# Performance work log

Measured on AMD Instinct MI355X. Metric: run time of the kernel, lower is better.

The kernel has to match this reference:

```python
import jax, jax.numpy as jnp
import numpy as np

N = 50000      # nodes
E = 800000     # edges (avg degree 16)
H = 128        # hidden_nf
NORM_FACTOR = 100.0   # normalization_factor, aggregation 'sum'
NORM_CONST = 1.0      # norm_constant (effective_constant = max(1, 1.0))
EPS = 1e-8


def silu(v):
    return v * jax.nn.sigmoid(v)


def setup_inputs() -> dict:
    key = jax.random.key(0)
    ks = jax.random.split(key, 16)
    IN_E = 2 * H + 2  # edge MLP input: h[row] | h[col] | [radial, edge_attr]

    def w(k, shape, scale=0.05):
        return jax.random.normal(k, shape, dtype=jnp.float32) * scale

    return {
        "h": jax.random.normal(ks[0], (N, H), dtype=jnp.float32),
        "x": jax.random.normal(ks[1], (N, 3), dtype=jnp.float32),
        "edge_index": jax.random.randint(ks[2], (2, E), 0, N, dtype=jnp.int32),
        "edge_attr": jax.random.normal(ks[3], (E, 1), dtype=jnp.float32),
        "node_mask": jnp.ones((N, 1), dtype=jnp.float32),
        "edge_mask": jnp.ones((E, 1), dtype=jnp.float32),
        # 2 stacked GCL layers (identical shapes -> stacked on leading dim)
        "gcl_e_w1": w(ks[4], (2, IN_E, H)), "gcl_e_b1": jnp.zeros((2, H), jnp.float32),
        "gcl_e_w2": w(ks[5], (2, H, H)),    "gcl_e_b2": jnp.zeros((2, H), jnp.float32),
        "gcl_a_w":  w(ks[6], (2, H, 1)),    "gcl_a_b":  jnp.zeros((2, 1), jnp.float32),
        "gcl_n_w1": w(ks[7], (2, 2 * H, H)),"gcl_n_b1": jnp.zeros((2, H), jnp.float32),
        "gcl_n_w2": w(ks[8], (2, H, H)),    "gcl_n_b2": jnp.zeros((2, H), jnp.float32),
        # EquivariantUpdate coord MLP (last layer xavier gain 0.001 -> tiny, no bias)
        "c_w1": w(ks[9], (IN_E, H)), "c_b1": jnp.zeros((H,), jnp.float32),
        "c_w2": w(ks[10], (H, H)),   "c_b2": jnp.zeros((H,), jnp.float32),
        "c_w3": w(ks[11], (H, 1), 0.001),
    }


def reference(h, x, edge_index, edge_attr, node_mask, edge_mask,
              gcl_e_w1, gcl_e_b1, gcl_e_w2, gcl_e_b2, gcl_a_w, gcl_a_b,
              gcl_n_w1, gcl_n_b1, gcl_n_w2, gcl_n_b2,
              c_w1, c_b1, c_w2, c_b2, c_w3):
    row, col = edge_index[0], edge_index[1]
    n_nodes = h.shape[0]

    # coord2diff
    diff = x[row] - x[col]                                  # [E,3]
    radial = jnp.sum(diff * diff, axis=1, keepdims=True)    # [E,1]
    norm = jnp.sqrt(radial + EPS)
    coord_diff = diff / (norm + NORM_CONST)

    # edge_attr = cat([distances, edge_attr])  -> edge_feat_nf = 2
    ea = jnp.concatenate([radial, edge_attr], axis=1)       # [E,2]

    # n_layers=2 GCLs with attention
    for i in range(2):
        einp = jnp.concatenate([h[row], h[col], ea], axis=1)             # [E,258]
        mij = silu(silu(einp @ gcl_e_w1[i] + gcl_e_b1[i]) @ gcl_e_w2[i] + gcl_e_b2[i])
        att = jax.nn.sigmoid(mij @ gcl_a_w[i] + gcl_a_b[i])
        ef = mij * att * edge_mask                                       # [E,H]
        agg = jax.ops.segment_sum(ef, row, num_segments=n_nodes) / NORM_FACTOR
        ninp = jnp.concatenate([h, agg], axis=1)                         # [N,2H]
        h = h + (silu(ninp @ gcl_n_w1[i] + gcl_n_b1[i]) @ gcl_n_w2[i] + gcl_n_b2[i])
        h = h * node_mask

    # EquivariantUpdate (tanh=False, reflection_equiv=True -> no cross term)
    einp = jnp.concatenate([h[row], h[col], ea], axis=1)
    phi = silu(silu(einp @ c_w1 + c_b1) @ c_w2 + c_b2) @ c_w3            # [E,1]
    trans = coord_diff * phi * edge_mask                                 # [E,3]
    aggx = jax.ops.segment_sum(trans, row, num_segments=n_nodes) / NORM_FACTOR
    x = (x + aggx) * node_mask

    h = h * node_mask
    return (h, x)
```

## Files before the change

kernel.cpp:

```cpp
#include <hip/hip_runtime.h>
#include <hip/hip_bf16.h>
#include <math.h>
#include <string.h>

#define DEV __device__ __forceinline__

typedef __bf16 bf16;
typedef bf16 bf16x8 __attribute__((ext_vector_type(8)));
typedef bf16 bf16x2 __attribute__((ext_vector_type(2)));
typedef float f32x4 __attribute__((ext_vector_type(4)));
typedef float f32x2 __attribute__((ext_vector_type(2)));
typedef unsigned int uint;
typedef unsigned char uchar;
typedef unsigned short ushort;

constexpr int N_NODES = 50000;
constexpr int N_EDGES = 800000;
constexpr int H = 128;
constexpr int NB_SCAN = (N_NODES + 255) / 256;

DEV float fsilu(float x) { return x / (1.f + __expf(-x)); }
DEV float fsigmoid(float x) { return 1.f / (1.f + __expf(-x)); }


__global__ void transpose_pad_kernel(bf16* __restrict__ dst, const float* __restrict__ src,
                                     int K, int Nf, int KP) {
    int idx = blockIdx.x * 256 + threadIdx.x;
    if (idx >= Nf * KP) return;
    int n = idx / KP, k = idx - n * KP;
    dst[idx] = (k < K) ? (bf16)src[k * Nf + n] : (bf16)0.f;
}

__global__ void h_init_kernel(const float* __restrict__ h, float* __restrict__ h_cur, int n) {
    int i = blockIdx.x * 256 + threadIdx.x;
    if (i < n) h_cur[i] = h[i];
}

__global__ void out_h_kernel(const float* __restrict__ h_cur, const float* __restrict__ nmask,
                             float* __restrict__ out) {
    int i = blockIdx.x * 256 + threadIdx.x;
    if (i < N_NODES * H) out[i] = h_cur[i] * nmask[i >> 7];
}


__global__ void count_kernel(const int* __restrict__ ei, int* __restrict__ deg) {
    int e = blockIdx.x * 256 + threadIdx.x;
    if (e < N_EDGES) atomicAdd(&deg[ei[e]], 1);
}

__global__ void scan1_kernel(const int* __restrict__ deg, int* __restrict__ off,
                             int* __restrict__ bsum) {
    __shared__ int s[256];
    int t = threadIdx.x, i = blockIdx.x * 256 + t;
    int v = (i < N_NODES) ? deg[i] : 0;
    s[t] = v;
    __syncthreads();
#pragma unroll
    for (int st = 1; st < 256; st <<= 1) {
        int x = (t >= st) ? s[t - st] : 0;
        __syncthreads();
        s[t] += x;
        __syncthreads();
    }
    if (i < N_NODES) off[i] = s[t] - v;
    if (t == 255) bsum[blockIdx.x] = s[255];
}

__global__ void scan2_kernel(int* __restrict__ bsum) {
    __shared__ int s[256];
    int t = threadIdx.x;
    int v = (t < NB_SCAN) ? bsum[t] : 0;
    s[t] = v;
    __syncthreads();
#pragma unroll
    for (int st = 1; st < 256; st <<= 1) {
        int x = (t >= st) ? s[t - st] : 0;
        __syncthreads();
        s[t] += x;
        __syncthreads();
    }
    if (t < NB_SCAN) bsum[t] = s[t] - v;
}

__global__ void scan3_kernel(int* __restrict__ off, const int* __restrict__ bsum) {
    int i = blockIdx.x * 256 + threadIdx.x;
    if (i >= N_NODES) return;
    off[i] += bsum[blockIdx.x];
}

__global__ void fill2_kernel(const int* __restrict__ ei, const float* __restrict__ eattr,
                             const float* __restrict__ emask, int* __restrict__ off,
                             uint* __restrict__ rc_pm, bf16* __restrict__ eaem_pm) {
    int e = blockIdx.x * 256 + threadIdx.x;
    if (e >= N_EDGES) return;
    int r = ei[e], c = ei[N_EDGES + e];
    int slot = atomicAdd(&off[r], 1);
    rc_pm[slot] = ((uint)r << 16) | (uint)c;
    eaem_pm[(size_t)slot * 2 + 0] = (bf16)eattr[e];
    eaem_pm[(size_t)slot * 2 + 1] = (bf16)emask[e];
}

__global__ __launch_bounds__(256, 2) void pq_kernel(
    const float* __restrict__ h_cur, const bf16* __restrict__ w1t,
    const float* __restrict__ b1, bf16* __restrict__ P, bf16* __restrict__ Q) {
    __shared__ __align__(16) bf16 hs[64 * 128];
    int t = threadIdx.x, lane = t & 63, wv = t >> 6;
    int lr = lane & 15, lg = lane >> 4;
    int nbase = blockIdx.x * 64;

    {
        int nl = t >> 2, q = t & 3;
        int node = nbase + nl;
        if (node < N_NODES) {
            const float4* hr = (const float4*)(h_cur + (size_t)node * H);
#pragma unroll
            for (int c = 0; c < 4; ++c) {
                float4 v0 = hr[q * 8 + c * 2];
                float4 v1 = hr[q * 8 + c * 2 + 1];
                bf16x8 o;
                o[0] = (bf16)v0.x; o[1] = (bf16)v0.y; o[2] = (bf16)v0.z; o[3] = (bf16)v0.w;
                o[4] = (bf16)v1.x; o[5] = (bf16)v1.y; o[6] = (bf16)v1.z; o[7] = (bf16)v1.w;
                int sl = (q * 4 + c) ^ (nl & 7);
                *(bf16x8*)(hs + nl * 128 + sl * 8) = o;
            }
        } else {
#pragma unroll
            for (int c = 0; c < 4; ++c) {
                int sl = (q * 4 + c) ^ (nl & 7);
                *(bf16x8*)(hs + nl * 128 + sl * 8) = (bf16x8)(bf16)0.f;
            }
        }
    }
    __syncthreads();

    f32x4 aP[4][2], aQ[4][2];
#pragma unroll
    for (int er = 0; er < 4; ++er)
#pragma unroll
        for (int j = 0; j < 2; ++j) { aP[er][j] = (f32x4)0.f; aQ[er][j] = (f32x4)0.f; }

    const bf16* bp0 = w1t + (size_t)((wv * 2 + 0) * 16 + lr) * 256 + lg * 8;
    const bf16* bp1 = w1t + (size_t)((wv * 2 + 1) * 16 + lr) * 256 + lg * 8;
#pragma unroll
    for (int kk = 0; kk < 4; ++kk) {
        bf16x8 a[4];
#pragma unroll
        for (int er = 0; er < 4; ++er) {
            int sl = (kk * 4 + lg) ^ (lr & 7);
            a[er] = *(const bf16x8*)(hs + (er * 16 + lr) * 128 + sl * 8);
        }
        bf16x8 bP0 = *(const bf16x8*)(bp0 + kk * 32);
        bf16x8 bP1 = *(const bf16x8*)(bp1 + kk * 32);
        bf16x8 bQ0 = *(const bf16x8*)(bp0 + 128 + kk * 32);
        bf16x8 bQ1 = *(const bf16x8*)(bp1 + 128 + kk * 32);
#pragma unroll
        for (int er = 0; er < 4; ++er) {
            aP[er][0] = __builtin_amdgcn_mfma_f32_16x16x32_bf16(a[er], bP0, aP[er][0], 0, 0, 0);
            aP[er][1] = __builtin_amdgcn_mfma_f32_16x16x32_bf16(a[er], bP1, aP[er][1], 0, 0, 0);
            aQ[er][0] = __builtin_amdgcn_mfma_f32_16x16x32_bf16(a[er], bQ0, aQ[er][0], 0, 0, 0);
            aQ[er][1] = __builtin_amdgcn_mfma_f32_16x16x32_bf16(a[er], bQ1, aQ[er][1], 0, 0, 0);
        }
    }

    float bb0 = b1[(wv * 2 + 0) * 16 + lr];
    float bb1v = b1[(wv * 2 + 1) * 16 + lr];
#pragma unroll
    for (int er = 0; er < 4; ++er) {
#pragma unroll
        for (int j = 0; j < 2; ++j) {
            int feat = (wv * 2 + j) * 16 + lr;
            float bb = j ? bb1v : bb0;
#pragma unroll
            for (int r = 0; r < 4; ++r) {
                int node = nbase + er * 16 + lg * 4 + r;
                if (node < N_NODES) {
                    P[(size_t)node * H + feat] = (bf16)(aP[er][j][r] + bb);
                    Q[(size_t)node * H + feat] = (bf16)(aQ[er][j][r]);
                }
            }
        }
    }
}


__global__ __launch_bounds__(256) void gather_h_kernel(
    const uchar* __restrict__ ef, const int* __restrict__ off, bf16* __restrict__ agg_bf) {
    int t = threadIdx.x, lane = t & 63, wv = t >> 6;
    int n = blockIdx.x * 4 + wv;
    if (n >= N_NODES) return;
    int st = (n == 0) ? 0 : off[n - 1];
    int dg = off[n] - st;
    const uchar* bp = ef + (size_t)st * 128 + lane * 2;
    float s0 = 0.f, s1 = 0.f;
    for (int k = 0; k < dg; ++k) {
        uint v = *(const ushort*)(bp + (size_t)k * 128);
        f32x2 f = __builtin_amdgcn_cvt_pk_f32_fp8(v, false);
        s0 += f.x;
        s1 += f.y;
    }
    bf16x2 o;
    o[0] = (bf16)(s0 * 0.01f);
    o[1] = (bf16)(s1 * 0.01f);
    *(bf16x2*)(agg_bf + (size_t)n * H + lane * 2) = o;
}

__global__ __launch_bounds__(256) void gather_x_kernel(
    const float* __restrict__ trans, const int* __restrict__ off,
    const float* __restrict__ x, const float* __restrict__ nmask, float* __restrict__ outx) {
    int t = threadIdx.x, lane = t & 63, wv = t >> 6;
    int n = blockIdx.x * 4 + wv;
    if (n >= N_NODES) return;
    int st = (n == 0) ? 0 : off[n - 1];
    int dg = off[n] - st;
    float sx = 0.f, sy = 0.f, sz = 0.f;
    for (int k = lane; k < dg; k += 64) {
        const float* tp = trans + (size_t)(st + k) * 3;
        sx += tp[0];
        sy += tp[1];
        sz += tp[2];
    }
#pragma unroll
    for (int m = 1; m < 64; m <<= 1) {
        sx += __shfl_xor(sx, m);
        sy += __shfl_xor(sy, m);
        sz += __shfl_xor(sz, m);
    }
    if (lane == 0) {
        float nm = nmask[n];
        outx[n * 3 + 0] = (x[n * 3 + 0] + sx * 0.01f) * nm;
        outx[n * 3 + 1] = (x[n * 3 + 1] + sy * 0.01f) * nm;
        outx[n * 3 + 2] = (x[n * 3 + 2] + sz * 0.01f) * nm;
    }
}


template <int KCHUNKS, int ASTRIDE, int BSTRIDE>
DEV void wave_gemm(const bf16* A_lds, const bf16* __restrict__ Bt,
                   f32x4 (&acc)[4][2], int lr, int lg, int wv) {
#pragma unroll
    for (int kk = 0; kk < KCHUNKS; ++kk) {
        int ko = kk * 32 + lg * 8;
        bf16x8 a[4], b[2];
#pragma unroll
        for (int er = 0; er < 4; ++er)
            a[er] = *(const bf16x8*)(A_lds + (er * 16 + lr) * ASTRIDE + ko);
#pragma unroll
        for (int j = 0; j < 2; ++j)
            b[j] = *(const bf16x8*)(Bt + (size_t)((wv * 2 + j) * 16 + lr) * BSTRIDE + ko);
#pragma unroll
        for (int er = 0; er < 4; ++er)
#pragma unroll
            for (int j = 0; j < 2; ++j)
                acc[er][j] = __builtin_amdgcn_mfma_f32_16x16x32_bf16(a[er], b[j], acc[er][j], 0, 0, 0);
    }
}

DEV void epi_silu_store(const f32x4 (&acc)[4][2], const float* __restrict__ bias,
                        bf16* out_lds, int OSTRIDE, int lr, int lg, int wv) {
    float b0 = bias[(wv * 2 + 0) * 16 + lr];
    float b1 = bias[(wv * 2 + 1) * 16 + lr];
#pragma unroll
    for (int er = 0; er < 4; ++er) {
#pragma unroll
        for (int j = 0; j < 2; ++j) {
            float bb = j ? b1 : b0;
            int fcol = (wv * 2 + j) * 16 + lr;
#pragma unroll
            for (int r = 0; r < 4; ++r) {
                int rrow = er * 16 + lg * 4 + r;
                out_lds[rrow * OSTRIDE + fcol] = (bf16)fsilu(acc[er][j][r] + bb);
            }
        }
    }
}

DEV void epi_silu_store_swz(const f32x4 (&acc)[4][2], const float* __restrict__ bias,
                            bf16* out_lds, int lr, int lg, int wv) {
    float b0 = bias[(wv * 2 + 0) * 16 + lr];
    float b1 = bias[(wv * 2 + 1) * 16 + lr];
#pragma unroll
    for (int er = 0; er < 4; ++er) {
#pragma unroll
        for (int j = 0; j < 2; ++j) {
            float bb = j ? b1 : b0;
            int fcol = (wv * 2 + j) * 16 + lr;
#pragma unroll
            for (int r = 0; r < 4; ++r) {
                int rrow = er * 16 + lg * 4 + r;
                int sl = (fcol >> 3) ^ (rrow & 7);
                out_lds[rrow * 128 + sl * 8 + (fcol & 7)] = (bf16)fsilu(acc[er][j][r] + bb);
            }
        }
    }
}

template <int MODE>
__global__ __launch_bounds__(256, 8) void edge_kernel(
    const bf16* __restrict__ P, const bf16* __restrict__ Q,
    const uint* __restrict__ rc_pm, const bf16* __restrict__ eaem_pm,
    const float* __restrict__ xg,
    const float* __restrict__ w_r, const float* __restrict__ w_e,
    const bf16* __restrict__ w2t, const float* __restrict__ b2,
    const float* __restrict__ avec, const float* __restrict__ abias,
    uchar* __restrict__ efout, float* __restrict__ trans) {
    __shared__ __align__(16) bf16 T[64 * 128];
    __shared__ __align__(16) float wr_l[128];
    __shared__ __align__(16) float we_l[128];
    __shared__ float part_l[64];

    int t = threadIdx.x, lane = t & 63, wv = t >> 6;
    int lr = lane & 15, lg = lane >> 4;
    int ebase = blockIdx.x * 64;
    int el = t >> 2, q = t & 3;

    {
        int rsub = lane >> 4;
        int slot = lane & 15;
#pragma unroll
        for (int u = 0; u < 4; ++u) {
            int r = wv * 16 + u * 4 + rsub;
            uint rcs = rc_pm[ebase + r];
            int nc = (int)(rcs & 0xffffu);
            int sl = slot ^ (r & 7);
            const bf16* gpc = Q + (size_t)nc * H + sl * 8;
            __builtin_amdgcn_global_load_lds(
                (const __attribute__((address_space(1))) void*)gpc,
                (__attribute__((address_space(3))) void*)&T[(wv * 16 + u * 4) * 128],
                16, 0, 0);
        }
    }
    if (t < 128) {
        wr_l[t] = w_r[t];
    } else {
        we_l[t - 128] = w_e[t - 128];
    }

    uint rc = rc_pm[ebase + el];
    int rr = (int)(rc >> 16), cc = (int)(rc & 0xffffu);
    float dx = xg[rr * 3 + 0] - xg[cc * 3 + 0];
    float dy = xg[rr * 3 + 1] - xg[cc * 3 + 1];
    float dz = xg[rr * 3 + 2] - xg[cc * 3 + 2];
    float radial = dx * dx + dy * dy + dz * dz;
    uint eu = *(const uint*)(eaem_pm + (size_t)(ebase + el) * 2);
    bf16x2 ep = __builtin_bit_cast(bf16x2, eu);
    float eattr = (float)ep[0];
    float em = (float)ep[1];

    bf16x8 pvr[4];
    const bf16* Pp = P + (size_t)rr * H + q * 32;
#pragma unroll
    for (int c = 0; c < 4; ++c) pvr[c] = *(const bf16x8*)(Pp + c * 8);

    __syncthreads();

    f32x2 rad2 = {radial, radial};
    f32x2 ea2 = {eattr, eattr};
#pragma unroll
    for (int c = 0; c < 4; ++c) {
        int sl = (q * 4 + c) ^ (el & 7);
        bf16* ap = T + el * 128 + sl * 8;
        uint4 qu = __builtin_bit_cast(uint4, *(const bf16x8*)ap);
        uint4 pu = __builtin_bit_cast(uint4, pvr[c]);
        bf16x8 o;
#pragma unroll
        for (int k = 0; k < 4; ++k) {
            uint puk = (&pu.x)[k], quk = (&qu.x)[k];
            f32x2 p2 = {__uint_as_float(puk << 16), __uint_as_float(puk & 0xffff0000u)};
            f32x2 q2 = {__uint_as_float(quk << 16), __uint_as_float(quk & 0xffff0000u)};
            f32x2 w2 = *(const f32x2*)(wr_l + q * 32 + c * 8 + k * 2);
            f32x2 e2 = *(const f32x2*)(we_l + q * 32 + c * 8 + k * 2);
            f32x2 v = p2 + q2 + rad2 * w2 + ea2 * e2;
            o[2 * k + 0] = (bf16)fsilu(v.x);
            o[2 * k + 1] = (bf16)fsilu(v.y);
        }
        *(bf16x8*)ap = o;
    }
    __syncthreads();

    f32x4 acc2[4][2];
#pragma unroll
    for (int er = 0; er < 4; ++er)
#pragma unroll
        for (int j = 0; j < 2; ++j) acc2[er][j] = (f32x4)0.f;
    {
        const bf16* cp0 = w2t + (size_t)((wv * 2 + 0) * 16 + lr) * 128 + lg * 8;
        const bf16* cp1 = w2t + (size_t)((wv * 2 + 1) * 16 + lr) * 128 + lg * 8;
#pragma unroll
        for (int kk = 0; kk < 4; ++kk) {
            bf16x8 a[4], b[2];
            b[0] = *(const bf16x8*)(cp0 + kk * 32);
            b[1] = *(const bf16x8*)(cp1 + kk * 32);
#pragma unroll
            for (int er = 0; er < 4; ++er) {
                int sl = (kk * 4 + lg) ^ (lr & 7);
                a[er] = *(const bf16x8*)(T + (er * 16 + lr) * 128 + sl * 8);
            }
#pragma unroll
            for (int er = 0; er < 4; ++er)
#pragma unroll
                for (int j = 0; j < 2; ++j)
                    acc2[er][j] = __builtin_amdgcn_mfma_f32_16x16x32_bf16(a[er], b[j], acc2[er][j], 0, 0, 0);
        }
    }
    __syncthreads();

    epi_silu_store_swz(acc2, b2, T, lr, lg, wv);
    __syncthreads();

    {
        f32x4 dacc = (f32x4)0.f;
#pragma unroll
        for (int kk = 0; kk < 4; ++kk) {
            int sl = (kk * 4 + lg) ^ (lr & 7);
            bf16x8 a = *(const bf16x8*)(T + (wv * 16 + lr) * 128 + sl * 8);
            bf16x8 b = (bf16x8)(bf16)0.f;
            if (lr == 0) {
#pragma unroll
                for (int i = 0; i < 8; ++i) b[i] = (bf16)avec[kk * 32 + lg * 8 + i];
            }
            dacc = __builtin_amdgcn_mfma_f32_16x16x32_bf16(a, b, dacc, 0, 0, 0);
        }
        if (lr == 0) {
#pragma unroll
            for (int r = 0; r < 4; ++r) part_l[wv * 16 + lg * 4 + r] = dacc[r];
        }
    }
    __syncthreads();

    float part = part_l[el];

    if (MODE == 0) {
        float att = fsigmoid(part + abias[0]);
        float scale = att * em;
        f32x2 sc2 = {scale, scale};
        uchar* edst = efout + (size_t)(ebase + el) * 128 + q * 32;
#pragma unroll
        for (int cpair = 0; cpair < 2; ++cpair) {
            uint4 wout;
#pragma unroll
            for (int cc = 0; cc < 2; ++cc) {
                int c = cpair * 2 + cc;
                int sl = (q * 4 + c) ^ (el & 7);
                uint4 mu = __builtin_bit_cast(uint4, *(const bf16x8*)(T + el * 128 + sl * 8));
                uint w0 = 0, w1 = 0;
                {
                    uint m0 = (&mu.x)[0], m1 = (&mu.x)[1];
                    f32x2 a2 = f32x2{__uint_as_float(m0 << 16), __uint_as_float(m0 & 0xffff0000u)} * sc2;
                    f32x2 b2v = f32x2{__uint_as_float(m1 << 16), __uint_as_float(m1 & 0xffff0000u)} * sc2;
                    w0 = __builtin_amdgcn_cvt_pk_fp8_f32(a2.x, a2.y, w0, false);
                    w0 = __builtin_amdgcn_cvt_pk_fp8_f32(b2v.x, b2v.y, w0, true);
                }
                {
                    uint m2 = (&mu.x)[2], m3 = (&mu.x)[3];
                    f32x2 a2 = f32x2{__uint_as_float(m2 << 16), __uint_as_float(m2 & 0xffff0000u)} * sc2;
                    f32x2 b2v = f32x2{__uint_as_float(m3 << 16), __uint_as_float(m3 & 0xffff0000u)} * sc2;
                    w1 = __builtin_amdgcn_cvt_pk_fp8_f32(a2.x, a2.y, w1, false);
                    w1 = __builtin_amdgcn_cvt_pk_fp8_f32(b2v.x, b2v.y, w1, true);
                }
                (&wout.x)[cc * 2 + 0] = w0;
                (&wout.x)[cc * 2 + 1] = w1;
            }
            *(uint4*)(edst + cpair * 16) = wout;
        }
    } else {
        if (q == 0) {
            float inv = 1.f / (sqrtf(radial + 1e-8f) + 1.f);
            float s = part * em * inv;
            int sI = ebase + el;
            trans[sI * 3 + 0] = dx * s;
            trans[sI * 3 + 1] = dy * s;
            trans[sI * 3 + 2] = dz * s;
        }
    }
}

__global__ __launch_bounds__(256, 2) void node_kernel(
    float* __restrict__ h_cur, const bf16* __restrict__ agg_bf,
    const bf16* __restrict__ w1t, const float* __restrict__ b1,
    const bf16* __restrict__ w2t, const float* __restrict__ b2,
    const float* __restrict__ nmask) {
    constexpr int SRN = 264;
    constexpr int TRN = 136;
    __shared__ __align__(16) bf16 ninp[64 * SRN];
    __shared__ __align__(16) bf16 t1[64 * TRN];

    int t = threadIdx.x, lane = t & 63, wv = t >> 6;
    int lr = lane & 15, lg = lane >> 4;
    int nbase = blockIdx.x * 64;

    {
        int nl = t >> 2, q = t & 3;
        int node = nbase + nl;
        bf16* dst = ninp + nl * SRN;
        if (node < N_NODES) {
            const float4* hr = (const float4*)(h_cur + (size_t)node * H);
            const bf16* ar = agg_bf + (size_t)node * H;
#pragma unroll
            for (int pp = 0; pp < 8; ++pp) {
                int ch = pp * 4 + q;
                float4 v = hr[ch];
                dst[ch * 4 + 0] = (bf16)v.x; dst[ch * 4 + 1] = (bf16)v.y;
                dst[ch * 4 + 2] = (bf16)v.z; dst[ch * 4 + 3] = (bf16)v.w;
            }
#pragma unroll
            for (int pp = 0; pp < 4; ++pp) {
                int ch = pp * 4 + q;
                *(bf16x8*)(dst + 128 + ch * 8) = *(const bf16x8*)(ar + ch * 8);
            }
        } else {
#pragma unroll
            for (int pp = 0; pp < 8; ++pp) {
                int ch = pp * 4 + q;
#pragma unroll
                for (int k = 0; k < 4; ++k) {
                    dst[ch * 4 + k] = (bf16)0.f;
                    dst[128 + ch * 4 + k] = (bf16)0.f;
                }
            }
        }
    }
    __syncthreads();

    f32x4 acc[4][2];
#pragma unroll
    for (int er = 0; er < 4; ++er)
#pragma unroll
        for (int j = 0; j < 2; ++j) acc[er][j] = (f32x4)0.f;
    wave_gemm<8, SRN, 256>(ninp, w1t, acc, lr, lg, wv);
    epi_silu_store(acc, b1, t1, TRN, lr, lg, wv);
    __syncthreads();

    f32x4 acc2[4][2];
#pragma unroll
    for (int er = 0; er < 4; ++er)
#pragma unroll
        for (int j = 0; j < 2; ++j) acc2[er][j] = (f32x4)0.f;
    wave_gemm<4, TRN, 128>(t1, w2t, acc2, lr, lg, wv);

    float bb0 = b2[(wv * 2 + 0) * 16 + lr];
    float bb1 = b2[(wv * 2 + 1) * 16 + lr];
#pragma unroll
    for (int er = 0; er < 4; ++er) {
#pragma unroll
        for (int j = 0; j < 2; ++j) {
            float bb = j ? bb1 : bb0;
            int feat = (wv * 2 + j) * 16 + lr;
#pragma unroll
            for (int r = 0; r < 4; ++r) {
                int node = nbase + er * 16 + lg * 4 + r;
                if (node < N_NODES) {
                    size_t idx = (size_t)node * H + feat;
                    float nm = nmask[node];
                    h_cur[idx] = (h_cur[idx] + acc2[er][j][r] + bb) * nm;
                }
            }
        }
    }
}

extern "C" void kernel_launch(void* const* d_in, const int* in_sizes, int n_in,
                              void* d_out, int out_size, void* d_ws, size_t ws_size,
                              hipStream_t stream) {
    (void)in_sizes; (void)n_in; (void)out_size; (void)ws_size;
    const float* h_in  = (const float*)d_in[0];
    const float* x_in  = (const float*)d_in[1];
    const int*   ei    = (const int*)d_in[2];
    const float* eattr = (const float*)d_in[3];
    const float* nmask = (const float*)d_in[4];
    const float* emask = (const float*)d_in[5];
    const float* e_w1  = (const float*)d_in[6];
    const float* e_b1  = (const float*)d_in[7];
    const float* e_w2  = (const float*)d_in[8];
    const float* e_b2  = (const float*)d_in[9];
    const float* a_w   = (const float*)d_in[10];
    const float* a_b   = (const float*)d_in[11];
    const float* n_w1  = (const float*)d_in[12];
    const float* n_b1  = (const float*)d_in[13];
    const float* n_w2  = (const float*)d_in[14];
    const float* n_b2  = (const float*)d_in[15];
    const float* c_w1  = (const float*)d_in[16];
    const float* c_b1  = (const float*)d_in[17];
    const float* c_w2  = (const float*)d_in[18];
    const float* c_b2  = (const float*)d_in[19];
    const float* c_w3  = (const float*)d_in[20];
    float* out = (float*)d_out;

    char* p = (char*)d_ws;
    auto alloc = [&](size_t bytes) { char* r = p; p += (bytes + 255) & ~(size_t)255; return r; };
    float* h_cur  = (float*)alloc((size_t)N_NODES * H * 4);
    bf16*  Pb     = (bf16*) alloc((size_t)N_NODES * H * 2);
    bf16*  Qb     = (bf16*) alloc((size_t)N_NODES * H * 2);
    bf16*  agg_bf = Qb;
    uchar* ef     = (uchar*)alloc((size_t)N_EDGES * 128);
    float* trans  = (float*)ef;
    int*   deg    = (int*)  alloc((size_t)N_NODES * 4);
    int*   off    = (int*)  alloc((size_t)N_NODES * 4);
    int*   bsum   = (int*)  alloc((size_t)NB_SCAN * 4);
    uint*  rc_pm  = (uint*) alloc((size_t)N_EDGES * 4);
    bf16*  eaem_pm= (bf16*) alloc((size_t)N_EDGES * 2 * 2);
    bf16*  e_w1t  = (bf16*) alloc((size_t)2 * 128 * 256 * 2);
    bf16*  e_w2t  = (bf16*) alloc((size_t)2 * 128 * 128 * 2);
    bf16*  n_w1t  = (bf16*) alloc((size_t)2 * 128 * 256 * 2);
    bf16*  n_w2t  = (bf16*) alloc((size_t)2 * 128 * 128 * 2);
    bf16*  c_w1t  = (bf16*) alloc((size_t)128 * 256 * 2);
    bf16*  c_w2t  = (bf16*) alloc((size_t)128 * 128 * 2);

    auto tp = [&](bf16* dst, const float* src, int K, int KP) {
        int tot = 128 * KP;
        transpose_pad_kernel<<<(tot + 255) / 256, 256, 0, stream>>>(dst, src, K, 128, KP);
    };
    tp(e_w1t, e_w1, 258, 256);               tp(e_w1t + 128 * 256, e_w1 + 258 * 128, 258, 256);
    tp(e_w2t, e_w2, 128, 128);               tp(e_w2t + 128 * 128, e_w2 + 128 * 128, 128, 128);
    tp(n_w1t, n_w1, 256, 256);               tp(n_w1t + 128 * 256, n_w1 + 256 * 128, 256, 256);
    tp(n_w2t, n_w2, 128, 128);               tp(n_w2t + 128 * 128, n_w2 + 128 * 128, 128, 128);
    tp(c_w1t, c_w1, 258, 256);
    tp(c_w2t, c_w2, 128, 128);

    h_init_kernel<<<(N_NODES * H + 255) / 256, 256, 0, stream>>>(h_in, h_cur, N_NODES * H);

    hipMemsetAsync(deg, 0, (size_t)N_NODES * 4, stream);
    count_kernel<<<(N_EDGES + 255) / 256, 256, 0, stream>>>(ei, deg);
    scan1_kernel<<<NB_SCAN, 256, 0, stream>>>(deg, off, bsum);
    scan2_kernel<<<1, 256, 0, stream>>>(bsum);
    scan3_kernel<<<NB_SCAN, 256, 0, stream>>>(off, bsum);
    fill2_kernel<<<(N_EDGES + 255) / 256, 256, 0, stream>>>(
        ei, eattr, emask, off, rc_pm, eaem_pm);

    int ngrid = (N_NODES + 3) / 4;
    int pqgrid = (N_NODES + 63) / 64;
    for (int i = 0; i < 2; ++i) {
        pq_kernel<<<pqgrid, 256, 0, stream>>>(
            h_cur, e_w1t + (size_t)i * 128 * 256, e_b1 + i * H, Pb, Qb);
        edge_kernel<0><<<N_EDGES / 64, 256, 0, stream>>>(
            Pb, Qb, rc_pm, eaem_pm, x_in,
            e_w1 + (size_t)i * 258 * 128 + 256 * 128,
            e_w1 + (size_t)i * 258 * 128 + 257 * 128,
            e_w2t + (size_t)i * 128 * 128, e_b2 + i * H,
            a_w + i * H, a_b + i, ef, nullptr);
        gather_h_kernel<<<ngrid, 256, 0, stream>>>(ef, off, agg_bf);
        node_kernel<<<(N_NODES + 63) / 64, 256, 0, stream>>>(
            h_cur, agg_bf,
            n_w1t + (size_t)i * 128 * 256, n_b1 + i * H,
            n_w2t + (size_t)i * 128 * 128, n_b2 + i * H, nmask);
    }
    pq_kernel<<<pqgrid, 256, 0, stream>>>(h_cur, c_w1t, c_b1, Pb, Qb);
    edge_kernel<1><<<N_EDGES / 64, 256, 0, stream>>>(
        Pb, Qb, rc_pm, eaem_pm, x_in,
        c_w1 + 256 * 128, c_w1 + 257 * 128,
        c_w2t, c_b2, c_w3, nullptr, nullptr, trans);
    gather_x_kernel<<<ngrid, 256, 0, stream>>>(trans, off, x_in, nmask,
                                               out + (size_t)N_NODES * H);

    out_h_kernel<<<(N_NODES * H + 255) / 256, 256, 0, stream>>>(h_cur, nmask, out);
}
```

Baseline: 807.0 us.

## Defer attention scaling to gather, store unscaled fp8 messages and per-edge weights

The edge kernel now writes the fp8 messages before the attention dot product's barrier and stores the per-edge attention times mask times 1/100 as a separate float array. The gather kernel multiplies each message by that weight while summing. This takes one __syncthreads and the attention dependency off the critical path of the message store. It also switches the message store and the gather load to nontemporal hints. The cost is an extra 4-byte read and write per edge and a multiply in the gather. Because the fp8 values are now unscaled, quantization error and range change, which could affect accuracy.

Result: slower. 851.3 us (+5.5%).

```diff
diff --git a/kernel.cpp b/kernel.cpp
--- a/kernel.cpp
+++ b/kernel.cpp
@@ -11,6 +11,7 @@
 typedef float f32x4 __attribute__((ext_vector_type(4)));
 typedef float f32x2 __attribute__((ext_vector_type(2)));
 typedef unsigned int uint;
+typedef uint u32x4 __attribute__((ext_vector_type(4)));
 typedef unsigned char uchar;
 typedef unsigned short ushort;
 
@@ -184,23 +185,26 @@
 
 
 __global__ __launch_bounds__(256) void gather_h_kernel(
-    const uchar* __restrict__ ef, const int* __restrict__ off, bf16* __restrict__ agg_bf) {
+    const uchar* __restrict__ ef, const float* __restrict__ attw,
+    const int* __restrict__ off, bf16* __restrict__ agg_bf) {
     int t = threadIdx.x, lane = t & 63, wv = t >> 6;
     int n = blockIdx.x * 4 + wv;
     if (n >= N_NODES) return;
     int st = (n == 0) ? 0 : off[n - 1];
     int dg = off[n] - st;
     const uchar* bp = ef + (size_t)st * 128 + lane * 2;
+    const float* sp = attw + st;
     float s0 = 0.f, s1 = 0.f;
     for (int k = 0; k < dg; ++k) {
-        uint v = *(const ushort*)(bp + (size_t)k * 128);
+        uint v = __builtin_nontemporal_load((const ushort*)(bp + (size_t)k * 128));
+        float sc = sp[k];
         f32x2 f = __builtin_amdgcn_cvt_pk_f32_fp8(v, false);
-        s0 += f.x;
-        s1 += f.y;
+        s0 += f.x * sc;
+        s1 += f.y * sc;
     }
     bf16x2 o;
-    o[0] = (bf16)(s0 * 0.01f);
-    o[1] = (bf16)(s1 * 0.01f);
+    o[0] = (bf16)s0;
+    o[1] = (bf16)s1;
     *(bf16x2*)(agg_bf + (size_t)n * H + lane * 2) = o;
 }
 
@@ -302,7 +306,7 @@
     const float* __restrict__ w_r, const float* __restrict__ w_e,
     const bf16* __restrict__ w2t, const float* __restrict__ b2,
     const float* __restrict__ avec, const float* __restrict__ abias,
-    uchar* __restrict__ efout, float* __restrict__ trans) {
+    uchar* __restrict__ efout, float* __restrict__ attout, float* __restrict__ trans) {
     __shared__ __align__(16) bf16 T[64 * 128];
     __shared__ __align__(16) float wr_l[128];
     __shared__ __align__(16) float we_l[128];
@@ -359,12 +363,12 @@
     for (int c = 0; c < 4; ++c) {
         int sl = (q * 4 + c) ^ (el & 7);
         bf16* ap = T + el * 128 + sl * 8;
-        uint4 qu = __builtin_bit_cast(uint4, *(const bf16x8*)ap);
-        uint4 pu = __builtin_bit_cast(uint4, pvr[c]);
+        u32x4 qu = __builtin_bit_cast(u32x4, *(const bf16x8*)ap);
+        u32x4 pu = __builtin_bit_cast(u32x4, pvr[c]);
         bf16x8 o;
 #pragma unroll
         for (int k = 0; k < 4; ++k) {
-            uint puk = (&pu.x)[k], quk = (&qu.x)[k];
+            uint puk = pu[k], quk = qu[k];
             f32x2 p2 = {__uint_as_float(puk << 16), __uint_as_float(puk & 0xffff0000u)};
             f32x2 q2 = {__uint_as_float(quk << 16), __uint_as_float(quk & 0xffff0000u)};
             f32x2 w2 = *(const f32x2*)(wr_l + q * 32 + c * 8 + k * 2);
@@ -407,63 +411,65 @@
     epi_silu_store_swz(acc2, b2, T, lr, lg, wv);
     __syncthreads();
 
-    {
-        f32x4 dacc = (f32x4)0.f;
-#pragma unroll
-        for (int kk = 0; kk < 4; ++kk) {
-            int sl = (kk * 4 + lg) ^ (lr & 7);
-            bf16x8 a = *(const bf16x8*)(T + (wv * 16 + lr) * 128 + sl * 8);
-            bf16x8 b = (bf16x8)(bf16)0.f;
-            if (lr == 0) {
-#pragma unroll
-                for (int i = 0; i < 8; ++i) b[i] = (bf16)avec[kk * 32 + lg * 8 + i];
-            }
-            dacc = __builtin_amdgcn_mfma_f32_16x16x32_bf16(a, b, dacc, 0, 0, 0);
-        }
+    f32x4 dacc = (f32x4)0.f;
+#pragma unroll
+    for (int kk = 0; kk < 4; ++kk) {
+        int sl = (kk * 4 + lg) ^ (lr & 7);
+        bf16x8 a = *(const bf16x8*)(T + (wv * 16 + lr) * 128 + sl * 8);
+        bf16x8 b = (bf16x8)(bf16)0.f;
         if (lr == 0) {
 #pragma unroll
-            for (int r = 0; r < 4; ++r) part_l[wv * 16 + lg * 4 + r] = dacc[r];
-        }
-    }
-    __syncthreads();
-
-    float part = part_l[el];
+            for (int i = 0; i < 8; ++i) b[i] = (bf16)avec[kk * 32 + lg * 8 + i];
+        }
+        dacc = __builtin_amdgcn_mfma_f32_16x16x32_bf16(a, b, dacc, 0, 0, 0);
+    }
 
     if (MODE == 0) {
-        float att = fsigmoid(part + abias[0]);
-        float scale = att * em;
-        f32x2 sc2 = {scale, scale};
         uchar* edst = efout + (size_t)(ebase + el) * 128 + q * 32;
 #pragma unroll
         for (int cpair = 0; cpair < 2; ++cpair) {
-            uint4 wout;
+            u32x4 wout;
 #pragma unroll
             for (int cc = 0; cc < 2; ++cc) {
                 int c = cpair * 2 + cc;
                 int sl = (q * 4 + c) ^ (el & 7);
-                uint4 mu = __builtin_bit_cast(uint4, *(const bf16x8*)(T + el * 128 + sl * 8));
+                u32x4 mu = __builtin_bit_cast(u32x4, *(const bf16x8*)(T + el * 128 + sl * 8));
                 uint w0 = 0, w1 = 0;
                 {
-                    uint m0 = (&mu.x)[0], m1 = (&mu.x)[1];
-                    f32x2 a2 = f32x2{__uint_as_float(m0 << 16), __uint_as_float(m0 & 0xffff0000u)} * sc2;
-                    f32x2 b2v = f32x2{__uint_as_float(m1 << 16), __uint_as_float(m1 & 0xffff0000u)} * sc2;
-                    w0 = __builtin_amdgcn_cvt_pk_fp8_f32(a2.x, a2.y, w0, false);
-                    w0 = __builtin_amdgcn_cvt_pk_fp8_f32(b2v.x, b2v.y, w0, true);
+                    uint m0 = mu[0], m1 = mu[1];
+                    w0 = __builtin_amdgcn_cvt_pk_fp8_f32(
+                        __uint_as_float(m0 << 16), __uint_as_float(m0 & 0xffff0000u), w0, false);
+                    w0 = __builtin_amdgcn_cvt_pk_fp8_f32(
+                        __uint_as_float(m1 << 16), __uint_as_float(m1 & 0xffff0000u), w0, true);
                 }
                 {
-                    uint m2 = (&mu.x)[2], m3 = (&mu.x)[3];
-                    f32x2 a2 = f32x2{__uint_as_float(m2 << 16), __uint_as_float(m2 & 0xffff0000u)} * sc2;
-                    f32x2 b2v = f32x2{__uint_as_float(m3 << 16), __uint_as_float(m3 & 0xffff0000u)} * sc2;
-                    w1 = __builtin_amdgcn_cvt_pk_fp8_f32(a2.x, a2.y, w1, false);
-                    w1 = __builtin_amdgcn_cvt_pk_fp8_f32(b2v.x, b2v.y, w1, true);
+                    uint m2 = mu[2], m3 = mu[3];
+                    w1 = __builtin_amdgcn_cvt_pk_fp8_f32(
+                        __uint_as_float(m2 << 16), __uint_as_float(m2 & 0xffff0000u), w1, false);
+                    w1 = __builtin_amdgcn_cvt_pk_fp8_f32(
+                        __uint_as_float(m3 << 16), __uint_as_float(m3 & 0xffff0000u), w1, true);
                 }
-                (&wout.x)[cc * 2 + 0] = w0;
-                (&wout.x)[cc * 2 + 1] = w1;
-            }
-            *(uint4*)(edst + cpair * 16) = wout;
+                wout[cc * 2 + 0] = w0;
+                wout[cc * 2 + 1] = w1;
+            }
+            __builtin_nontemporal_store(wout, (u32x4*)(edst + cpair * 16));
+        }
+    }
+
+    if (lr == 0) {
+#pragma unroll
+        for (int r = 0; r < 4; ++r) part_l[wv * 16 + lg * 4 + r] = dacc[r];
+    }
+    __syncthreads();
+
+    if (MODE == 0) {
+        if (q == 0) {
+            float part = part_l[el];
+            attout[ebase + el] = fsigmoid(part + abias[0]) * em * 0.01f;
         }
     } else {
         if (q == 0) {
+            float part = part_l[el];
             float inv = 1.f / (sqrtf(radial + 1e-8f) + 1.f);
             float s = part * em * inv;
             int sI = ebase + el;
@@ -593,6 +599,7 @@
     bf16*  agg_bf = Qb;
     uchar* ef     = (uchar*)alloc((size_t)N_EDGES * 128);
     float* trans  = (float*)ef;
+    float* attw   = (float*)alloc((size_t)N_EDGES * 4);
     int*   deg    = (int*)  alloc((size_t)N_NODES * 4);
     int*   off    = (int*)  alloc((size_t)N_NODES * 4);
     int*   bsum   = (int*)  alloc((size_t)NB_SCAN * 4);
@@ -636,8 +643,8 @@
             e_w1 + (size_t)i * 258 * 128 + 256 * 128,
             e_w1 + (size_t)i * 258 * 128 + 257 * 128,
             e_w2t + (size_t)i * 128 * 128, e_b2 + i * H,
-            a_w + i * H, a_b + i, ef, nullptr);
-        gather_h_kernel<<<ngrid, 256, 0, stream>>>(ef, off, agg_bf);
+            a_w + i * H, a_b + i, ef, attw, nullptr);
+        gather_h_kernel<<<ngrid, 256, 0, stream>>>(ef, attw, off, agg_bf);
         node_kernel<<<(N_NODES + 63) / 64, 256, 0, stream>>>(
             h_cur, agg_bf,
             n_w1t + (size_t)i * 128 * 256, n_b1 + i * H,
@@ -647,7 +654,7 @@
     edge_kernel<1><<<N_EDGES / 64, 256, 0, stream>>>(
         Pb, Qb, rc_pm, eaem_pm, x_in,
         c_w1 + 256 * 128, c_w1 + 257 * 128,
-        c_w2t, c_b2, c_w3, nullptr, nullptr, trans);
+        c_w2t, c_b2, c_w3, nullptr, nullptr, nullptr, trans);
     gather_x_kernel<<<ngrid, 256, 0, stream>>>(trans, off, x_in, nmask,
                                                out + (size_t)N_NODES * H);
 
```
